# Performance work log

Hardware: AMD Instinct MI355X
Metric: run time of the kernel (lower is better)

## Reference

```python
import jax, jax.numpy as jnp
import numpy as np

B, T, DP, A = 1024, 256, 64, 8   # batch, num particles (seq len), particle dim, action dim
H = 256                          # recurr_size (GRU hidden)
HID = 256                        # MLP hidden
C = 2                            # num_critics
TIME_NORM = 100.0


def setup_inputs() -> dict:
    key = jax.random.key(0)
    ks = jax.random.split(key, 10)
    F = DP + 1        # features + weight channel
    DIN = H + A + 1   # encoding + action + time
    s = lambda k, shape: (jax.random.normal(k, shape, jnp.float32) * 0.05)
    return {
        "particles": jax.random.normal(ks[0], (B, T, DP), jnp.float32),
        "weights": jax.random.uniform(ks[1], (B, T), jnp.float32),
        "action": jax.random.normal(ks[2], (B, A), jnp.float32),
        "time_idx": jax.random.uniform(ks[3], (B,), jnp.float32) * TIME_NORM,
        # GRU params (flax GRUCell layout, gates fused as [r|z|n]):
        "Wi": s(ks[4], (F, 3 * H)),    # input kernel (ir|iz|in), with bias
        "bi": jnp.zeros((3 * H,), jnp.float32),
        "Wh": s(ks[5], (H, 3 * H)),    # hidden kernel (hr|hz|hn); only hn has bias
        "bhn": jnp.zeros((H,), jnp.float32),
        # Two MLPDecoder critics stacked on leading dim C:
        "W1": s(ks[6], (C, DIN, HID)),
        "b1": jnp.zeros((C, HID), jnp.float32),
        "W2": s(ks[7], (C, HID, HID)),
        "b2": jnp.zeros((C, HID), jnp.float32),
        "W3": s(ks[8], (C, HID, 1)),
        "b3": jnp.zeros((C, 1), jnp.float32),
    }


def reference(particles, weights, action, time_idx, Wi, bi, Wh, bhn, W1, b1, W2, b2, W3, b3):
    # feature_fn = identity; append particle weights as an extra channel
    inputs = jnp.concatenate([particles, weights[..., None]], axis=-1)  # [B,T,F]
    # Precompute all input projections (parallel over time), scan only the recurrence.
    xp = jnp.einsum('btf,fg->btg', inputs, Wi) + bi                     # [B,T,3H]
    xp = jnp.swapaxes(xp, 0, 1)                                         # [T,B,3H]
    h0 = jnp.zeros((inputs.shape[0], H), inputs.dtype)

    def step(h, x):
        hp = h @ Wh                                                     # [B,3H]
        r = jax.nn.sigmoid(x[:, :H] + hp[:, :H])
        z = jax.nn.sigmoid(x[:, H:2 * H] + hp[:, H:2 * H])
        n = jnp.tanh(x[:, 2 * H:] + r * (hp[:, 2 * H:] + bhn))
        h_new = (1.0 - z) * n + z * h
        return h_new, None

    h, _ = jax.lax.scan(step, h0, xp)                                   # last encoding [B,H]

    t = (time_idx / TIME_NORM)[:, None]                                 # [B,1]
    x = jnp.concatenate([h, action, t], axis=-1)                        # [B,DIN]

    # Both critic MLPs batched over leading critic dim C (ReLU hidden layers).
    h1 = jax.nn.relu(jnp.einsum('bd,cdh->cbh', x, W1) + b1[:, None, :])   # [C,B,HID]
    h2 = jax.nn.relu(jnp.einsum('cbh,chk->cbk', h1, W2) + b2[:, None, :]) # [C,B,HID]
    v = jnp.einsum('cbh,cho->cbo', h2, W3) + b3[:, None, :]               # [C,B,1]
    return jnp.moveaxis(v[..., 0], 0, -1)                               # [B,C]
```

## Files before the change

### kernel.cpp

```cpp
#include <hip/hip_runtime.h>


#define TSEQ 256
#define DPDIM 64

typedef float f32x4 __attribute__((ext_vector_type(4)));
typedef __bf16 bf16x8 __attribute__((ext_vector_type(8)));
typedef unsigned short ushort8 __attribute__((ext_vector_type(8)));

static __device__ __forceinline__ unsigned short f2bf(float f) {
  unsigned u = __builtin_bit_cast(unsigned, f);
  return (unsigned short)((u + 0x7fffu + ((u >> 16) & 1u)) >> 16);
}
static __device__ __forceinline__ float bf2f(unsigned short h) {
  return __builtin_bit_cast(float, ((unsigned)h) << 16);
}
static __device__ __forceinline__ float sigm(float x) {
  return __builtin_amdgcn_rcpf(1.f + __expf(-x));
}
static __device__ __forceinline__ float tanh_fast(float p) {
  float q = __expf(-2.f * fabsf(p));
  float t = (1.f - q) * __builtin_amdgcn_rcpf(1.f + q);
  return __builtin_bit_cast(float, __builtin_bit_cast(unsigned, t) |
                                   (__builtin_bit_cast(unsigned, p) & 0x80000000u));
}

#define OFF_WIT 0
#define OFF_XP  110592
#define OFF_H0  135168
#define OFF_H1  137888
#define OFF_BI  140608
#define OFF_W64 143680
#define LDS_GRU 146752

#define HSTRIDE 544

__global__ __launch_bounds__(512, 2) void gru_kernel(
    const float* __restrict__ particles, const float* __restrict__ weights,
    const float* __restrict__ Wi, const float* __restrict__ bi,
    const float* __restrict__ Wh, const float* __restrict__ bhn,
    unsigned short* __restrict__ hT)
{
  extern __shared__ char smem[];
  const int tid  = threadIdx.x;
  const int lane = tid & 63;
  const int w    = tid >> 6;
  const int l15  = lane & 15;
  const int kg   = lane >> 4;
  const int b0   = blockIdx.x * 4;

  for (int idx = tid; idx < 64 * 768; idx += 512) {
    int k = idx / 768, n = idx - k * 768;
    *(unsigned short*)(smem + OFF_WIT + n * 144 + k * 2) = f2bf(Wi[idx]);
  }
  for (int idx = tid; idx < 768; idx += 512) {
    *(float*)(smem + OFF_BI  + idx * 4) = bi[idx];
    *(float*)(smem + OFF_W64 + idx * 4) = Wi[64 * 768 + idx];
  }
  for (int idx = tid; idx < (2 * 5 * HSTRIDE) / 4; idx += 512)
    ((unsigned*)(smem + OFF_H0))[idx] = 0u;

  const int hcol0 = w * 16 + l15;
  const float bhn0 = bhn[hcol0];
  const float bhn1 = bhn[hcol0 + 128];

  bf16x8 whb[6][8];
  #pragma unroll
  for (int j = 0; j < 6; ++j) {
    const int tile = w + 8 * j;
    const float* wp = Wh + (size_t)(kg * 8) * 768 + tile * 16 + l15;
    #pragma unroll
    for (int ks = 0; ks < 8; ++ks) {
      ushort8 tmp;
      #pragma unroll
      for (int e = 0; e < 8; ++e)
        tmp[e] = f2bf(wp[(size_t)(ks * 32 + e) * 768]);
      whb[j][ks] = __builtin_bit_cast(bf16x8, tmp);
    }
  }
  __syncthreads();

  const unsigned arow = ((l15 & 3) == 0)
                      ? (unsigned)((l15 >> 2) * HSTRIDE + kg * 16)
                      : (unsigned)(4 * HSTRIDE + kg * 16);

  const float* pbase = particles +
      ((size_t)(b0 + (l15 >> 2)) * TSEQ + (l15 & 3)) * DPDIM + kg * 8;
  const float* wbase = weights + (size_t)(b0 + kg) * TSEQ;

  char* const xpb = smem + OFF_XP + hcol0 * 32 + kg * 8;

  f32x4 acc[6];
  const f32x4 fzero = {0.f, 0.f, 0.f, 0.f};
  float hreg0 = 0.f, hreg1 = 0.f;

  for (int g = 0; g < 64; ++g) {
    const int t0 = g * 4;

    #pragma unroll
    for (int j = 0; j < 6; ++j) acc[j] = fzero;
    #pragma unroll
    for (int ks = 0; ks < 2; ++ks) {
      const float* pp = pbase + (size_t)t0 * DPDIM + ks * 32;
      f32x4 pa = *(const f32x4*)pp;
      f32x4 pb = *(const f32x4*)(pp + 4);
      ushort8 tmp;
      tmp[0] = f2bf(pa[0]); tmp[1] = f2bf(pa[1]); tmp[2] = f2bf(pa[2]); tmp[3] = f2bf(pa[3]);
      tmp[4] = f2bf(pb[0]); tmp[5] = f2bf(pb[1]); tmp[6] = f2bf(pb[2]); tmp[7] = f2bf(pb[3]);
      bf16x8 af = __builtin_bit_cast(bf16x8, tmp);
      #pragma unroll
      for (int j = 0; j < 6; ++j) {
        const int n = hcol0 + 128 * j;
        bf16x8 bf = *(const bf16x8*)(smem + OFF_WIT + n * 144 + ks * 64 + kg * 16);
        acc[j] = __builtin_amdgcn_mfma_f32_16x16x32_bf16(af, bf, acc[j], 0, 0, 0);
      }
    }
    {
      f32x4 wv = *(const f32x4*)(wbase + t0);
      #pragma unroll
      for (int j = 0; j < 6; ++j) {
        const int col = hcol0 + 128 * j;
        const float biv  = *(const float*)(smem + OFF_BI  + col * 4);
        const float w64v = *(const float*)(smem + OFF_W64 + col * 4);
        float v0 = acc[j][0] + biv + wv[0] * w64v;
        float v1 = acc[j][1] + biv + wv[1] * w64v;
        float v2 = acc[j][2] + biv + wv[2] * w64v;
        float v3 = acc[j][3] + biv + wv[3] * w64v;
        uint2 val;
        val.x = (unsigned)f2bf(v0) | ((unsigned)f2bf(v1) << 16);
        val.y = (unsigned)f2bf(v2) | ((unsigned)f2bf(v3) << 16);
        *(uint2*)(xpb + j * 4096) = val;
      }
    }

    #pragma unroll
    for (int tt = 0; tt < 4; ++tt) {
      const int t     = t0 + tt;
      const int rboff = (t & 1) ? OFF_H1 : OFF_H0;
      const int wboff = (t & 1) ? OFF_H0 : OFF_H1;
      #pragma unroll
      for (int j = 0; j < 6; ++j) acc[j] = fzero;
      const char* hb = smem + rboff;
      #pragma unroll
      for (int ks = 0; ks < 8; ++ks) {
        bf16x8 af = *(const bf16x8*)(hb + arow + ks * 64);
        #pragma unroll
        for (int j = 0; j < 6; ++j)
          acc[j] = __builtin_amdgcn_mfma_f32_16x16x32_bf16(af, whb[j][ks], acc[j], 0, 0, 0);
      }
      float xr0 = bf2f(*(const unsigned short*)(xpb + 0 * 4096 + tt * 2));
      float xr1 = bf2f(*(const unsigned short*)(xpb + 1 * 4096 + tt * 2));
      float xz0 = bf2f(*(const unsigned short*)(xpb + 2 * 4096 + tt * 2));
      float xz1 = bf2f(*(const unsigned short*)(xpb + 3 * 4096 + tt * 2));
      float xn0 = bf2f(*(const unsigned short*)(xpb + 4 * 4096 + tt * 2));
      float xn1 = bf2f(*(const unsigned short*)(xpb + 5 * 4096 + tt * 2));
      float rr0 = sigm(xr0 + acc[0][0]);
      float zz0 = sigm(xz0 + acc[2][0]);
      float nn0 = tanh_fast(xn0 + rr0 * (acc[4][0] + bhn0));
      unsigned short h0u = f2bf(nn0 + zz0 * (hreg0 - nn0));
      hreg0 = bf2f(h0u);
      float rr1 = sigm(xr1 + acc[1][0]);
      float zz1 = sigm(xz1 + acc[3][0]);
      float nn1 = tanh_fast(xn1 + rr1 * (acc[5][0] + bhn1));
      unsigned short h1u = f2bf(nn1 + zz1 * (hreg1 - nn1));
      hreg1 = bf2f(h1u);
      *(unsigned short*)(smem + wboff + kg * HSTRIDE + hcol0 * 2)         = h0u;
      *(unsigned short*)(smem + wboff + kg * HSTRIDE + (hcol0 + 128) * 2) = h1u;
      __syncthreads();
    }
  }

  hT[(size_t)(b0 + kg) * 256 + hcol0]       = f2bf(hreg0);
  hT[(size_t)(b0 + kg) * 256 + hcol0 + 128] = f2bf(hreg1);
}

#define HOFF_XA 0
#define HOFF_B  37888
#define HOFF_H1 58368
#define HOFF_H2 92160
#define HOFF_B1 125952
#define HOFF_B2 126976
#define HOFF_W3 128000
#define LDS_HEAD 129024

__global__ __launch_bounds__(256, 2) void head_kernel(
    const unsigned short* __restrict__ hT, const float* __restrict__ action,
    const float* __restrict__ time_idx, const float* __restrict__ W1,
    const float* __restrict__ b1, const float* __restrict__ W2,
    const float* __restrict__ b2, const float* __restrict__ W3,
    const float* __restrict__ b3, float* __restrict__ out)
{
  extern __shared__ char smem[];
  const int tid  = threadIdx.x;
  const int lane = tid & 63;
  const int w    = tid >> 6;
  const int l15  = lane & 15;
  const int kg   = lane >> 4;
  const int c    = blockIdx.x & 1;
  const int rt   = blockIdx.x >> 1;
  const int r0   = rt * 64;

  if (tid < 256) {
    *(float*)(smem + HOFF_B1 + tid * 4) = b1[c * 256 + tid];
    *(float*)(smem + HOFF_B2 + tid * 4) = b2[c * 256 + tid];
    *(float*)(smem + HOFF_W3 + tid * 4) = W3[c * 256 + tid];
  }
  for (int idx = tid; idx < 64 * 296; idx += 256) {
    int row = idx / 296, k = idx - row * 296;
    unsigned short v;
    if (k < 256)       v = hT[(r0 + row) * 256 + k];
    else if (k < 264)  v = f2bf(action[(r0 + row) * 8 + (k - 256)]);
    else if (k == 264) v = f2bf(time_idx[r0 + row] * 0.01f);
    else               v = 0;
    *(unsigned short*)(smem + HOFF_XA + row * 592 + k * 2) = v;
  }

  f32x4 acc[4][4];
  const f32x4 fzero = {0.f, 0.f, 0.f, 0.f};

  #pragma unroll
  for (int mt = 0; mt < 4; ++mt)
    #pragma unroll
    for (int i = 0; i < 4; ++i) acc[mt][i] = fzero;
  for (int ks = 0; ks < 9; ++ks) {
    for (int idx = tid; idx < 32 * 256; idx += 256) {
      int kk = idx >> 8, n = idx & 255;
      int kglob = ks * 32 + kk;
      float v = (kglob < 265) ? W1[((size_t)c * 265 + kglob) * 256 + n] : 0.f;
      *(unsigned short*)(smem + HOFF_B + n * 80 + kk * 2) = f2bf(v);
    }
    __syncthreads();
    bf16x8 bfr[4];
    #pragma unroll
    for (int i = 0; i < 4; ++i)
      bfr[i] = *(const bf16x8*)(smem + HOFF_B + ((w * 4 + i) * 16 + l15) * 80 + kg * 16);
    #pragma unroll
    for (int mt = 0; mt < 4; ++mt) {
      bf16x8 af = *(const bf16x8*)(smem + HOFF_XA + (mt * 16 + l15) * 592 + ks * 64 + kg * 16);
      #pragma unroll
      for (int i = 0; i < 4; ++i)
        acc[mt][i] = __builtin_amdgcn_mfma_f32_16x16x32_bf16(af, bfr[i], acc[mt][i], 0, 0, 0);
    }
    __syncthreads();
  }
  #pragma unroll
  for (int mt = 0; mt < 4; ++mt)
    #pragma unroll
    for (int i = 0; i < 4; ++i) {
      int col = (w * 4 + i) * 16 + l15;
      float bv = *(const float*)(smem + HOFF_B1 + col * 4);
      #pragma unroll
      for (int r = 0; r < 4; ++r) {
        float v = acc[mt][i][r] + bv; v = v > 0.f ? v : 0.f;
        *(unsigned short*)(smem + HOFF_H1 + (mt * 16 + kg * 4 + r) * 528 + col * 2) = f2bf(v);
      }
    }
  __syncthreads();

  #pragma unroll
  for (int mt = 0; mt < 4; ++mt)
    #pragma unroll
    for (int i = 0; i < 4; ++i) acc[mt][i] = fzero;
  for (int ks = 0; ks < 8; ++ks) {
    for (int idx = tid; idx < 32 * 256; idx += 256) {
      int kk = idx >> 8, n = idx & 255;
      float v = W2[((size_t)c * 256 + ks * 32 + kk) * 256 + n];
      *(unsigned short*)(smem + HOFF_B + n * 80 + kk * 2) = f2bf(v);
    }
    __syncthreads();
    bf16x8 bfr[4];
    #pragma unroll
    for (int i = 0; i < 4; ++i)
      bfr[i] = *(const bf16x8*)(smem + HOFF_B + ((w * 4 + i) * 16 + l15) * 80 + kg * 16);
    #pragma unroll
    for (int mt = 0; mt < 4; ++mt) {
      bf16x8 af = *(const bf16x8*)(smem + HOFF_H1 + (mt * 16 + l15) * 528 + ks * 64 + kg * 16);
      #pragma unroll
      for (int i = 0; i < 4; ++i)
        acc[mt][i] = __builtin_amdgcn_mfma_f32_16x16x32_bf16(af, bfr[i], acc[mt][i], 0, 0, 0);
    }
    __syncthreads();
  }
  #pragma unroll
  for (int mt = 0; mt < 4; ++mt)
    #pragma unroll
    for (int i = 0; i < 4; ++i) {
      int col = (w * 4 + i) * 16 + l15;
      float bv = *(const float*)(smem + HOFF_B2 + col * 4);
      #pragma unroll
      for (int r = 0; r < 4; ++r) {
        float v = acc[mt][i][r] + bv; v = v > 0.f ? v : 0.f;
        *(unsigned short*)(smem + HOFF_H2 + (mt * 16 + kg * 4 + r) * 528 + col * 2) = f2bf(v);
      }
    }
  __syncthreads();

  {
    int row = tid >> 2, q = tid & 3;
    float s = 0.f;
    #pragma unroll
    for (int i = 0; i < 16; ++i) {
      uint2 hh = *(const uint2*)(smem + HOFF_H2 + row * 528 + (q * 64 + i * 4) * 2);
      const float* w3p = (const float*)(smem + HOFF_W3) + q * 64 + i * 4;
      s += bf2f((unsigned short)hh.x)         * w3p[0];
      s += bf2f((unsigned short)(hh.x >> 16)) * w3p[1];
      s += bf2f((unsigned short)hh.y)         * w3p[2];
      s += bf2f((unsigned short)(hh.y >> 16)) * w3p[3];
    }
    s += __shfl_xor(s, 1);
    s += __shfl_xor(s, 2);
    if (q == 0) out[(r0 + row) * 2 + c] = s + b3[c];
  }
}

extern "C" void kernel_launch(void* const* d_in, const int* in_sizes, int n_in,
                              void* d_out, int out_size, void* d_ws, size_t ws_size,
                              hipStream_t stream) {
  const float* particles = (const float*)d_in[0];
  const float* weights   = (const float*)d_in[1];
  const float* action    = (const float*)d_in[2];
  const float* time_idx  = (const float*)d_in[3];
  const float* Wi        = (const float*)d_in[4];
  const float* bi        = (const float*)d_in[5];
  const float* Wh        = (const float*)d_in[6];
  const float* bhn       = (const float*)d_in[7];
  const float* W1        = (const float*)d_in[8];
  const float* b1        = (const float*)d_in[9];
  const float* W2        = (const float*)d_in[10];
  const float* b2        = (const float*)d_in[11];
  const float* W3        = (const float*)d_in[12];
  const float* b3        = (const float*)d_in[13];
  unsigned short* hT = (unsigned short*)d_ws;
  float* out = (float*)d_out;

  (void)hipFuncSetAttribute((const void*)gru_kernel,
                            hipFuncAttributeMaxDynamicSharedMemorySize, LDS_GRU);
  (void)hipFuncSetAttribute((const void*)head_kernel,
                            hipFuncAttributeMaxDynamicSharedMemorySize, LDS_HEAD);

  hipLaunchKernelGGL(gru_kernel, dim3(256), dim3(512), LDS_GRU, stream,
                     particles, weights, Wi, bi, Wh, bhn, hT);
  hipLaunchKernelGGL(head_kernel, dim3(32), dim3(256), LDS_HEAD, stream,
                     hT, action, time_idx, W1, b1, W2, b2, W3, b3, out);
}
```

Baseline: 752.0 us.

## Keep input projections in registers, fold biases into MFMA accumulators, split head rows

The GRU kernel now keeps the per-group input projections packed as bf16 in registers instead of round-tripping them through LDS. It also seeds the MFMA accumulators with the bias, weight-channel and x terms so the gate adds come for free. The recurrent A-fragment loads are double-buffered, restricted to the lanes that need them, and wrapped in raised wave priority. The head kernel processes 32 rows per block with twice as many blocks to spread work across more CUs. The risks are higher register pressure from the packed values and a slightly different rounding order for the input projection.

```diff
diff --git a/kernel.cpp b/kernel.cpp
--- a/kernel.cpp
+++ b/kernel.cpp
@@ -14,6 +14,14 @@
 }
 static __device__ __forceinline__ float bf2f(unsigned short h) {
   return __builtin_bit_cast(float, ((unsigned)h) << 16);
+}
+static __device__ __forceinline__ unsigned pk2(float a, float b) {
+  return (unsigned)f2bf(a) | ((unsigned)f2bf(b) << 16);
+}
+static __device__ __forceinline__ float upk(uint2 v, int tt) {
+  unsigned u = (tt & 2) ? v.y : v.x;
+  return (tt & 1) ? __builtin_bit_cast(float, u & 0xffff0000u)
+                  : __builtin_bit_cast(float, u << 16);
 }
 static __device__ __forceinline__ float sigm(float x) {
   return __builtin_amdgcn_rcpf(1.f + __expf(-x));
@@ -26,12 +34,11 @@
 }
 
 #define OFF_WIT 0
-#define OFF_XP  110592
-#define OFF_H0  135168
-#define OFF_H1  137888
-#define OFF_BI  140608
-#define OFF_W64 143680
-#define LDS_GRU 146752
+#define OFF_H0  110592
+#define OFF_H1  112768
+#define OFF_BI  114944
+#define OFF_W64 118016
+#define LDS_GRU 121088
 
 #define HSTRIDE 544
 
@@ -57,7 +64,7 @@
     *(float*)(smem + OFF_BI  + idx * 4) = bi[idx];
     *(float*)(smem + OFF_W64 + idx * 4) = Wi[64 * 768 + idx];
   }
-  for (int idx = tid; idx < (2 * 5 * HSTRIDE) / 4; idx += 512)
+  for (int idx = tid; idx < (2 * 4 * HSTRIDE) / 4; idx += 512)
     ((unsigned*)(smem + OFF_H0))[idx] = 0u;
 
   const int hcol0 = w * 16 + l15;
@@ -80,25 +87,38 @@
   }
   __syncthreads();
 
-  const unsigned arow = ((l15 & 3) == 0)
-                      ? (unsigned)((l15 >> 2) * HSTRIDE + kg * 16)
-                      : (unsigned)(4 * HSTRIDE + kg * 16);
+  const bool lm = (l15 & 3) == 0;
+  const unsigned arow = (unsigned)((l15 >> 2) * HSTRIDE + kg * 16);
 
   const float* pbase = particles +
       ((size_t)(b0 + (l15 >> 2)) * TSEQ + (l15 & 3)) * DPDIM + kg * 8;
   const float* wbase = weights + (size_t)(b0 + kg) * TSEQ;
 
-  char* const xpb = smem + OFF_XP + hcol0 * 32 + kg * 8;
-
   f32x4 acc[6];
+  uint2 xpk[6];
   const f32x4 fzero = {0.f, 0.f, 0.f, 0.f};
+  #pragma unroll
+  for (int j = 0; j < 6; ++j) acc[j] = fzero;
+  bf16x8 af0 = __builtin_bit_cast(bf16x8, (ushort8){0,0,0,0,0,0,0,0});
+  bf16x8 af1 = af0;
   float hreg0 = 0.f, hreg1 = 0.f;
 
   for (int g = 0; g < 64; ++g) {
     const int t0 = g * 4;
 
-    #pragma unroll
-    for (int j = 0; j < 6; ++j) acc[j] = fzero;
+    {
+      f32x4 wv = *(const f32x4*)(wbase + t0);
+      #pragma unroll
+      for (int j = 0; j < 6; ++j) {
+        const int col = hcol0 + 128 * j;
+        const float biv  = *(const float*)(smem + OFF_BI  + col * 4);
+        const float w64v = *(const float*)(smem + OFF_W64 + col * 4);
+        acc[j][0] = biv + wv[0] * w64v;
+        acc[j][1] = biv + wv[1] * w64v;
+        acc[j][2] = biv + wv[2] * w64v;
+        acc[j][3] = biv + wv[3] * w64v;
+      }
+    }
     #pragma unroll
     for (int ks = 0; ks < 2; ++ks) {
       const float* pp = pbase + (size_t)t0 * DPDIM + ks * 32;
@@ -115,22 +135,10 @@
         acc[j] = __builtin_amdgcn_mfma_f32_16x16x32_bf16(af, bf, acc[j], 0, 0, 0);
       }
     }
-    {
-      f32x4 wv = *(const f32x4*)(wbase + t0);
-      #pragma unroll
-      for (int j = 0; j < 6; ++j) {
-        const int col = hcol0 + 128 * j;
-        const float biv  = *(const float*)(smem + OFF_BI  + col * 4);
-        const float w64v = *(const float*)(smem + OFF_W64 + col * 4);
-        float v0 = acc[j][0] + biv + wv[0] * w64v;
-        float v1 = acc[j][1] + biv + wv[1] * w64v;
-        float v2 = acc[j][2] + biv + wv[2] * w64v;
-        float v3 = acc[j][3] + biv + wv[3] * w64v;
-        uint2 val;
-        val.x = (unsigned)f2bf(v0) | ((unsigned)f2bf(v1) << 16);
-        val.y = (unsigned)f2bf(v2) | ((unsigned)f2bf(v3) << 16);
-        *(uint2*)(xpb + j * 4096) = val;
-      }
+    #pragma unroll
+    for (int j = 0; j < 6; ++j) {
+      xpk[j].x = pk2(acc[j][0], acc[j][1]);
+      xpk[j].y = pk2(acc[j][2], acc[j][3]);
     }
 
     #pragma unroll
@@ -138,30 +146,37 @@
       const int t     = t0 + tt;
       const int rboff = (t & 1) ? OFF_H1 : OFF_H0;
       const int wboff = (t & 1) ? OFF_H0 : OFF_H1;
-      #pragma unroll
-      for (int j = 0; j < 6; ++j) acc[j] = fzero;
+      acc[0][0] = upk(xpk[0], tt);
+      acc[1][0] = upk(xpk[1], tt);
+      acc[2][0] = upk(xpk[2], tt);
+      acc[3][0] = upk(xpk[3], tt);
+      acc[4][0] = bhn0;
+      acc[5][0] = bhn1;
       const char* hb = smem + rboff;
-      #pragma unroll
-      for (int ks = 0; ks < 8; ++ks) {
-        bf16x8 af = *(const bf16x8*)(hb + arow + ks * 64);
+      __builtin_amdgcn_s_setprio(1);
+      if (lm) af0 = *(const bf16x8*)(hb + arow);
+      #pragma unroll
+      for (int ks = 0; ks < 8; ks += 2) {
+        if (lm) af1 = *(const bf16x8*)(hb + arow + (ks + 1) * 64);
         #pragma unroll
         for (int j = 0; j < 6; ++j)
-          acc[j] = __builtin_amdgcn_mfma_f32_16x16x32_bf16(af, whb[j][ks], acc[j], 0, 0, 0);
-      }
-      float xr0 = bf2f(*(const unsigned short*)(xpb + 0 * 4096 + tt * 2));
-      float xr1 = bf2f(*(const unsigned short*)(xpb + 1 * 4096 + tt * 2));
-      float xz0 = bf2f(*(const unsigned short*)(xpb + 2 * 4096 + tt * 2));
-      float xz1 = bf2f(*(const unsigned short*)(xpb + 3 * 4096 + tt * 2));
-      float xn0 = bf2f(*(const unsigned short*)(xpb + 4 * 4096 + tt * 2));
-      float xn1 = bf2f(*(const unsigned short*)(xpb + 5 * 4096 + tt * 2));
-      float rr0 = sigm(xr0 + acc[0][0]);
-      float zz0 = sigm(xz0 + acc[2][0]);
-      float nn0 = tanh_fast(xn0 + rr0 * (acc[4][0] + bhn0));
+          acc[j] = __builtin_amdgcn_mfma_f32_16x16x32_bf16(af0, whb[j][ks], acc[j], 0, 0, 0);
+        if (ks + 2 < 8) { if (lm) af0 = *(const bf16x8*)(hb + arow + (ks + 2) * 64); }
+        #pragma unroll
+        for (int j = 0; j < 6; ++j)
+          acc[j] = __builtin_amdgcn_mfma_f32_16x16x32_bf16(af1, whb[j][ks + 1], acc[j], 0, 0, 0);
+      }
+      __builtin_amdgcn_s_setprio(0);
+      float xn0v = upk(xpk[4], tt);
+      float xn1v = upk(xpk[5], tt);
+      float rr0 = sigm(acc[0][0]);
+      float zz0 = sigm(acc[2][0]);
+      float nn0 = tanh_fast(xn0v + rr0 * acc[4][0]);
       unsigned short h0u = f2bf(nn0 + zz0 * (hreg0 - nn0));
       hreg0 = bf2f(h0u);
-      float rr1 = sigm(xr1 + acc[1][0]);
-      float zz1 = sigm(xz1 + acc[3][0]);
-      float nn1 = tanh_fast(xn1 + rr1 * (acc[5][0] + bhn1));
+      float rr1 = sigm(acc[1][0]);
+      float zz1 = sigm(acc[3][0]);
+      float nn1 = tanh_fast(xn1v + rr1 * acc[5][0]);
       unsigned short h1u = f2bf(nn1 + zz1 * (hreg1 - nn1));
       hreg1 = bf2f(h1u);
       *(unsigned short*)(smem + wboff + kg * HSTRIDE + hcol0 * 2)         = h0u;
@@ -182,6 +197,8 @@
 #define HOFF_B2 126976
 #define HOFF_W3 128000
 #define LDS_HEAD 129024
+
+#define HROWS 32
 
 __global__ __launch_bounds__(256, 2) void head_kernel(
     const unsigned short* __restrict__ hT, const float* __restrict__ action,
@@ -198,14 +215,14 @@
   const int kg   = lane >> 4;
   const int c    = blockIdx.x & 1;
   const int rt   = blockIdx.x >> 1;
-  const int r0   = rt * 64;
+  const int r0   = rt * HROWS;
 
   if (tid < 256) {
     *(float*)(smem + HOFF_B1 + tid * 4) = b1[c * 256 + tid];
     *(float*)(smem + HOFF_B2 + tid * 4) = b2[c * 256 + tid];
     *(float*)(smem + HOFF_W3 + tid * 4) = W3[c * 256 + tid];
   }
-  for (int idx = tid; idx < 64 * 296; idx += 256) {
+  for (int idx = tid; idx < HROWS * 296; idx += 256) {
     int row = idx / 296, k = idx - row * 296;
     unsigned short v;
     if (k < 256)       v = hT[(r0 + row) * 256 + k];
@@ -215,11 +232,11 @@
     *(unsigned short*)(smem + HOFF_XA + row * 592 + k * 2) = v;
   }
 
-  f32x4 acc[4][4];
+  f32x4 acc[2][4];
   const f32x4 fzero = {0.f, 0.f, 0.f, 0.f};
 
   #pragma unroll
-  for (int mt = 0; mt < 4; ++mt)
+  for (int mt = 0; mt < 2; ++mt)
     #pragma unroll
     for (int i = 0; i < 4; ++i) acc[mt][i] = fzero;
   for (int ks = 0; ks < 9; ++ks) {
@@ -235,7 +252,7 @@
     for (int i = 0; i < 4; ++i)
       bfr[i] = *(const bf16x8*)(smem + HOFF_B + ((w * 4 + i) * 16 + l15) * 80 + kg * 16);
     #pragma unroll
-    for (int mt = 0; mt < 4; ++mt) {
+    for (int mt = 0; mt < 2; ++mt) {
       bf16x8 af = *(const bf16x8*)(smem + HOFF_XA + (mt * 16 + l15) * 592 + ks * 64 + kg * 16);
       #pragma unroll
       for (int i = 0; i < 4; ++i)
@@ -244,7 +261,7 @@
     __syncthreads();
   }
   #pragma unroll
-  for (int mt = 0; mt < 4; ++mt)
+  for (int mt = 0; mt < 2; ++mt)
     #pragma unroll
     for (int i = 0; i < 4; ++i) {
       int col = (w * 4 + i) * 16 + l15;
@@ -258,7 +275,7 @@
   __syncthreads();
 
   #pragma unroll
-  for (int mt = 0; mt < 4; ++mt)
+  for (int mt = 0; mt < 2; ++mt)
     #pragma unroll
     for (int i = 0; i < 4; ++i) acc[mt][i] = fzero;
   for (int ks = 0; ks < 8; ++ks) {
@@ -273,7 +290,7 @@
     for (int i = 0; i < 4; ++i)
       bfr[i] = *(const bf16x8*)(smem + HOFF_B + ((w * 4 + i) * 16 + l15) * 80 + kg * 16);
     #pragma unroll
-    for (int mt = 0; mt < 4; ++mt) {
+    for (int mt = 0; mt < 2; ++mt) {
       bf16x8 af = *(const bf16x8*)(smem + HOFF_H1 + (mt * 16 + l15) * 528 + ks * 64 + kg * 16);
       #pragma unroll
       for (int i = 0; i < 4; ++i)
@@ -282,7 +299,7 @@
     __syncthreads();
   }
   #pragma unroll
-  for (int mt = 0; mt < 4; ++mt)
+  for (int mt = 0; mt < 2; ++mt)
     #pragma unroll
     for (int i = 0; i < 4; ++i) {
       int col = (w * 4 + i) * 16 + l15;
@@ -297,19 +314,21 @@
 
   {
     int row = tid >> 2, q = tid & 3;
-    float s = 0.f;
-    #pragma unroll
-    for (int i = 0; i < 16; ++i) {
-      uint2 hh = *(const uint2*)(smem + HOFF_H2 + row * 528 + (q * 64 + i * 4) * 2);
-      const float* w3p = (const float*)(smem + HOFF_W3) + q * 64 + i * 4;
-      s += bf2f((unsigned short)hh.x)         * w3p[0];
-      s += bf2f((unsigned short)(hh.x >> 16)) * w3p[1];
-      s += bf2f((unsigned short)hh.y)         * w3p[2];
-      s += bf2f((unsigned short)(hh.y >> 16)) * w3p[3];
-    }
-    s += __shfl_xor(s, 1);
-    s += __shfl_xor(s, 2);
-    if (q == 0) out[(r0 + row) * 2 + c] = s + b3[c];
+    if (row < HROWS) {
+      float s = 0.f;
+      #pragma unroll
+      for (int i = 0; i < 16; ++i) {
+        uint2 hh = *(const uint2*)(smem + HOFF_H2 + row * 528 + (q * 64 + i * 4) * 2);
+        const float* w3p = (const float*)(smem + HOFF_W3) + q * 64 + i * 4;
+        s += bf2f((unsigned short)hh.x)         * w3p[0];
+        s += bf2f((unsigned short)(hh.x >> 16)) * w3p[1];
+        s += bf2f((unsigned short)hh.y)         * w3p[2];
+        s += bf2f((unsigned short)(hh.y >> 16)) * w3p[3];
+      }
+      s += __shfl_xor(s, 1);
+      s += __shfl_xor(s, 2);
+      if (q == 0) out[(r0 + row) * 2 + c] = s + b3[c];
+    }
   }
 }
 
@@ -340,6 +359,6 @@
 
   hipLaunchKernelGGL(gru_kernel, dim3(256), dim3(512), LDS_GRU, stream,
                      particles, weights, Wi, bi, Wh, bhn, hT);
-  hipLaunchKernelGGL(head_kernel, dim3(32), dim3(256), LDS_HEAD, stream,
+  hipLaunchKernelGGL(head_kernel, dim3(64), dim3(256), LDS_HEAD, stream,
                      hT, action, time_idx, W1, b1, W2, b2, W3, b3, out);
 }
```

Measured after the change: 842.5 us. 1.12x slower.
